# Kernel tuning notes

Measured on AMD Instinct MI355X. Metric: run time of the kernel, lower is better.

## Reference

```python
import jax, jax.numpy as jnp
import numpy as np
import math

F_FEATS = 51
BATCH = 256
N_WINDOW = 10
W_IN = N_WINDOW - 1          # input_window = 9
BUCKET = 6
EMB = 6
HEADS = 3
DHEAD = EMB // HEADS
FFN = 12
TOP_M = 80
HID = F_FEATS * EMB          # 306


def _layernorm(x, s, b, eps=1e-5):
    mu = jnp.mean(x, -1, keepdims=True)
    var = jnp.var(x, -1, keepdims=True)
    return (x - mu) / jnp.sqrt(var + eps) * s + b


def setup_inputs() -> dict:
    key = jax.random.key(0)
    ks = jax.random.split(key, 32)
    g = lambda i, shape, sc=0.1: jax.random.normal(ks[i], shape, dtype=jnp.float32) * sc
    inp = {
        "src": jax.random.uniform(ks[0], (N_WINDOW, BATCH, F_FEATS), dtype=jnp.float32),
        "tgt": jax.random.uniform(ks[1], (N_WINDOW, BATCH, F_FEATS), dtype=jnp.float32),
        # AutoDis params, batched over features (torch loops over n_feats modules)
        "w1_w": g(2, (F_FEATS, BUCKET), 0.5),          # Linear(1,bs) weight squeezed
        "w1_b": g(3, (F_FEATS, BUCKET)),
        "w2_w": g(4, (F_FEATS, BUCKET, BUCKET), 0.3),  # torch layout (out,in)
        "w2_b": g(5, (F_FEATS, BUCKET)),
        "meta": g(6, (F_FEATS, BUCKET, EMB), 0.5),     # EmbeddingBag table per feature
        # Sparse top-m MHSA (1 layer, post-norm encoder)
        "Wq": g(7, (EMB, EMB), 0.3), "bq": g(8, (EMB,)),
        "Wk": g(9, (EMB, EMB), 0.3), "bk": g(10, (EMB,)),
        "Wv": g(11, (EMB, EMB), 0.3), "bv": g(12, (EMB,)),
        "Wo": g(13, (EMB, EMB), 0.3), "bo": g(14, (EMB,)),
        "ln1_s": jnp.ones((EMB,), jnp.float32), "ln1_b": jnp.zeros((EMB,), jnp.float32),
        "ffn_w1": g(15, (FFN, EMB), 0.3), "ffn_b1": g(16, (FFN,)),
        "ffn_w2": g(17, (EMB, FFN), 0.3), "ffn_b2": g(18, (EMB,)),
        "ln2_s": jnp.ones((EMB,), jnp.float32), "ln2_b": jnp.zeros((EMB,), jnp.float32),
        # GRU (1 layer), torch gate order r,z,n
        "gru_wih": g(19, (3 * HID, HID), 0.05),
        "gru_whh": g(20, (3 * HID, HID), 0.05),
        "gru_bih": g(21, (3 * HID,)),
        "gru_bhh": g(22, (3 * HID,)),
        "h0": g(23, (1, BATCH, HID), 1.0),             # init_hidden
        # final FCN
        "fcn_w": g(24, (F_FEATS, HID), 0.05),
        "fcn_b": g(25, (F_FEATS,)),
    }
    return inp


def reference(src, tgt, w1_w, w1_b, w2_w, w2_b, meta,
              Wq, bq, Wk, bk, Wv, bv, Wo, bo,
              ln1_s, ln1_b, ffn_w1, ffn_b1, ffn_w2, ffn_b2, ln2_s, ln2_b,
              gru_wih, gru_whh, gru_bih, gru_bhh, h0, fcn_w, fcn_b):
    s = src[:-1]                                  # [W=9, B, F]
    W, B, F = s.shape
    # ---- AutoDis, vectorized across all features (replaces per-feature loop) ----
    h1 = jax.nn.leaky_relu(s[..., None] * w1_w + w1_b)            # [W,B,F,6]
    h2 = jnp.einsum('wbfi,fji->wbfj', h1, w2_w) + w2_b            # Linear(bs,bs)
    probs = jax.nn.softmax((h2 + 0.5 * h1) / 1e-5, axis=-1)      # temperature 1e-5
    emb = jnp.einsum('wbfi,fie->wbfe', probs, meta)               # weighted EmbeddingBag sum
    # rearrange 'w b f e -> b (w f) e' and scale by sqrt(emb)
    x = emb.transpose(1, 0, 2, 3).reshape(B, W * F, EMB) * math.sqrt(EMB)
    # ---- Sparse top-m MHSA encoder layer (post-norm) ----
    T = W * F                                                     # 459 tokens
    def heads(t):
        return t.reshape(B, T, HEADS, DHEAD).transpose(0, 2, 1, 3)
    q = heads(x @ Wq.T + bq)
    k = heads(x @ Wk.T + bk)
    v = heads(x @ Wv.T + bv)
    scores = jnp.einsum('bhqd,bhkd->bhqk', q, k) / math.sqrt(DHEAD)
    kth = jax.lax.top_k(scores, TOP_M)[0][..., -1:]               # m-th largest per query
    scores = jnp.where(scores >= kth, scores, -jnp.inf)           # keep only top-m keys
    attn = jax.nn.softmax(scores, axis=-1)
    o = jnp.einsum('bhqk,bhkd->bhqd', attn, v).transpose(0, 2, 1, 3).reshape(B, T, EMB)
    x = _layernorm(x + (o @ Wo.T + bo), ln1_s, ln1_b)
    f = jax.nn.relu(x @ ffn_w1.T + ffn_b1) @ ffn_w2.T + ffn_b2
    x = _layernorm(x + f, ln2_s, ln2_b)
    # rearrange 'b (w f) e -> w b (f e)'
    seq = x.reshape(B, W, F, EMB).transpose(1, 0, 2, 3).reshape(W, B, F * EMB)
    # ---- GRU over seq[:-1] (8 steps) ----
    def step(h, xt):
        gi = xt @ gru_wih.T + gru_bih
        gh = h @ gru_whh.T + gru_bhh
        ir, iz, inn = jnp.split(gi, 3, -1)
        hr, hz, hn = jnp.split(gh, 3, -1)
        r = jax.nn.sigmoid(ir + hr)
        z = jax.nn.sigmoid(iz + hz)
        n = jnp.tanh(inn + r * hn)
        h = (1.0 - z) * n + z * h
        return h, None
    hT, _ = jax.lax.scan(step, h0[0, :B], seq[:-1])               # lstm_out[-1] == final hidden
    out = jax.nn.sigmoid(hT @ fcn_w.T + fcn_b)[None]              # [1, B, F]
    return out


if __name__ == '__main__':
    o = reference(**setup_inputs())
    print(o.shape)
```

## Files before the change

kernel.cpp:

```cpp
#include <hip/hip_runtime.h>
#include <math.h>

#define WWIN 9
#define BATCH 256
#define FEAT 51
#define TT 459
#define EMBD 6
#define HID 306
#define G3 918
#define FFND 12
#define TOPM 80
#define MAXTASK 320
#define NPAIR 153
#define NPAIR2 154
#define WSTRIDE 920

__device__ __forceinline__ float leakyf(float v){ return v >= 0.f ? v : 0.01f*v; }
__device__ __forceinline__ float sigmf(float v){ return 1.f/(1.f+__expf(-v)); }

__device__ __forceinline__ unsigned fkey(float s){
    unsigned fb = __float_as_uint(s);
    unsigned m = (unsigned)((int)fb >> 31);
    return fb ^ (m | 0x80000000u);
}
__device__ __forceinline__ float fkey_inv(unsigned k){
    unsigned fb = (k & 0x80000000u) ? (k ^ 0x80000000u) : ~k;
    return __uint_as_float(fb);
}
__device__ __forceinline__ unsigned bfrne(float f){
    unsigned u = __float_as_uint(f);
    u += 0x7fffu + ((u >> 16) & 1u);
    return u >> 16;
}

template<int CTRL, int RMASK>
__device__ __forceinline__ float dpp_add(float v){
    int r = __builtin_amdgcn_update_dpp(0, __float_as_int(v), CTRL, RMASK, 0xf, true);
    return v + __int_as_float(r);
}
__device__ __forceinline__ float wave_fsum(float v){
    v = dpp_add<0x111, 0xf>(v);
    v = dpp_add<0x112, 0xf>(v);
    v = dpp_add<0x114, 0xf>(v);
    v = dpp_add<0x118, 0xf>(v);
    v = dpp_add<0x142, 0xa>(v);
    v = dpp_add<0x143, 0xc>(v);
    return __int_as_float(__builtin_amdgcn_readlane(__float_as_int(v), 63));
}
template<int CTRL, int RMASK>
__device__ __forceinline__ unsigned dpp_uadd(unsigned v){
    unsigned r = (unsigned)__builtin_amdgcn_update_dpp(0, (int)v, CTRL, RMASK, 0xf, true);
    return v + r;
}
__device__ __forceinline__ unsigned wave_usum(unsigned v){
    v = dpp_uadd<0x111, 0xf>(v);
    v = dpp_uadd<0x112, 0xf>(v);
    v = dpp_uadd<0x114, 0xf>(v);
    v = dpp_uadd<0x118, 0xf>(v);
    v = dpp_uadd<0x142, 0xa>(v);
    v = dpp_uadd<0x143, 0xc>(v);
    return (unsigned)__builtin_amdgcn_readlane((int)v, 63);
}
template<int CTRL, int RMASK>
__device__ __forceinline__ unsigned dpp_min(unsigned v){
    unsigned r = (unsigned)__builtin_amdgcn_update_dpp((int)v, (int)v, CTRL, RMASK, 0xf, false);
    return v < r ? v : r;
}
__device__ __forceinline__ unsigned wave_umin(unsigned v){
    v = dpp_min<0x111, 0xf>(v);
    v = dpp_min<0x112, 0xf>(v);
    v = dpp_min<0x114, 0xf>(v);
    v = dpp_min<0x118, 0xf>(v);
    v = dpp_min<0x142, 0xa>(v);
    v = dpp_min<0x143, 0xc>(v);
    return (unsigned)__builtin_amdgcn_readlane((int)v, 63);
}

__global__ __launch_bounds__(512) void embed_tasks(
    const float* __restrict__ src,
    const float* __restrict__ w1w, const float* __restrict__ w1b,
    const float* __restrict__ w2w, const float* __restrict__ w2b,
    const float* __restrict__ meta,
    const float* __restrict__ Wq, const float* __restrict__ bq,
    const float* __restrict__ Wk, const float* __restrict__ bk,
    const float* __restrict__ Wv, const float* __restrict__ bv,
    const float* __restrict__ wih, const float* __restrict__ whh,
    const float* __restrict__ fcw,
    float* __restrict__ WIHT, unsigned* __restrict__ WHB, float* __restrict__ FCNT,
    float* __restrict__ X, float* __restrict__ Q,
    float* __restrict__ K, float* __restrict__ V,
    int* __restrict__ TASKS, int* __restrict__ ROWMAP, int* __restrict__ NT)
{
    __shared__ int sbuck[TT];
    int b = blockIdx.x;
    int t = threadIdx.x;

    for (int idx = blockIdx.x*512 + threadIdx.x; idx < G3*HID; idx += 256*512){
        int o = idx / HID, i = idx % HID;
        WIHT[i*G3 + o] = wih[idx];
    }
    for (int idx = blockIdx.x*512 + threadIdx.x; idx < NPAIR2*WSTRIDE; idx += 256*512){
        int p = idx / WSTRIDE, c = idx % WSTRIDE;
        unsigned v = 0u;
        if (c < G3 && p < NPAIR){
            unsigned lo = bfrne(whh[(size_t)c*HID + 2*p]);
            unsigned hi = bfrne(whh[(size_t)c*HID + 2*p + 1]);
            v = lo | (hi << 16);
        }
        WHB[idx] = v;
    }
    for (int idx = blockIdx.x*512 + threadIdx.x; idx < FEAT*HID; idx += 256*512){
        int f = idx / HID, i = idx % HID;
        FCNT[i*FEAT + f] = fcw[idx];
    }

    if (t < TT){
        int w = t / FEAT, f = t % FEAT;
        float s = src[(w*BATCH + b)*FEAT + f];
        float h1[EMBD], h2[EMBD];
        #pragma unroll
        for (int i=0;i<EMBD;i++) h1[i] = leakyf(s*w1w[f*EMBD+i] + w1b[f*EMBD+i]);
        #pragma unroll
        for (int j=0;j<EMBD;j++){
            float a = 0.f;
            #pragma unroll
            for (int i=0;i<EMBD;i++) a += h1[i]*w2w[(f*EMBD+j)*EMBD+i];
            h2[j] = a + w2b[f*EMBD+j];
        }
        float z[EMBD];
        float m = -INFINITY; int jm = 0;
        #pragma unroll
        for (int j=0;j<EMBD;j++){
            z[j] = (h2[j] + 0.5f*h1[j]) * 1e+05f;
            if (z[j] > m){ m = z[j]; jm = j; }
        }
        float se = 0.f;
        #pragma unroll
        for (int j=0;j<EMBD;j++){ z[j] = expf(z[j]-m); se += z[j]; }
        float inv = 1.0f / se;
        #pragma unroll
        for (int j=0;j<EMBD;j++) z[j] *= inv;
        sbuck[t] = jm;

        float xr[EMBD];
        #pragma unroll
        for (int e=0;e<EMBD;e++){
            float a = 0.f;
            #pragma unroll
            for (int i=0;i<EMBD;i++) a += z[i]*meta[(f*EMBD+i)*EMBD+e];
            xr[e] = a * 2.449489742783178f;
        }
        float* xp = X + (b*TT + t)*EMBD;
        float* qp = Q + (b*TT + t)*EMBD;
        float* kp = K + (b*TT + t)*EMBD;
        float* vp = V + (b*TT + t)*EMBD;
        #pragma unroll
        for (int e=0;e<EMBD;e++){
            xp[e] = xr[e];
            float aq=0.f, ak=0.f, av=0.f;
            #pragma unroll
            for (int i=0;i<EMBD;i++){
                aq += xr[i]*Wq[e*EMBD+i];
                ak += xr[i]*Wk[e*EMBD+i];
                av += xr[i]*Wv[e*EMBD+i];
            }
            qp[e] = aq + bq[e];
            kp[e] = ak + bk[e];
            vp[e] = av + bv[e];
        }
    }
    __syncthreads();
    if (threadIdx.x < 64){
        int f = threadIdx.x;
        unsigned mask = 0; unsigned cnts = 0; int repw[6]; int cnt = 0;
        if (f < FEAT){
            #pragma unroll
            for (int w=0; w<WWIN; w++){
                int j = sbuck[w*FEAT + f];
                if (!((mask>>j) & 1u)){ mask |= 1u<<j; repw[j] = w; }
                cnts += 1u << (5*j);
            }
            cnt = __popc(mask);
        }
        int inc = cnt;
        #pragma unroll
        for (int off=1; off<64; off<<=1){
            int n = __shfl_up(inc, off, 64);
            if (threadIdx.x >= off) inc += n;
        }
        int offset = inc - cnt;
        if (f < FEAT){
            int rk = 0;
            #pragma unroll
            for (int j=0;j<6;j++){
                if ((mask>>j) & 1u){
                    int mult = (int)((cnts >> (5*j)) & 31u);
                    TASKS[b*MAXTASK + offset + rk] =
                        (mult<<13) | (f<<7) | (j<<4) | repw[j];
                    rk++;
                }
            }
            #pragma unroll
            for (int w=0;w<WWIN;w++){
                int j = sbuck[w*FEAT + f];
                int r = __popc(mask & ((1u<<j)-1u));
                ROWMAP[b*TT + w*FEAT + f] = offset + r;
            }
        }
        if (threadIdx.x == 63) NT[b] = inc;
    }
}

__global__ __launch_bounds__(256) void attn_topk(
    const float* __restrict__ Q, const float* __restrict__ K,
    const float* __restrict__ V, const int* __restrict__ TASKS,
    const int* __restrict__ NT, float2* __restrict__ OD)
{
    int blk = blockIdx.x;
    int b = blk / 3, h = blk % 3;
    const int base = b*TT*EMBD + 2*h;
    int wave = threadIdx.x >> 6, lane = threadIdx.x & 63;
    int nt = NT[b];

    float rkx[4], rky[4], rvx[4], rvy[4], rmf[4];
    unsigned rpm[4];
    #pragma unroll
    for (int s=0;s<4;s++){
        int tix = lane + (s<<6);
        rkx[s]=0.f; rky[s]=0.f; rvx[s]=0.f; rvy[s]=0.f; rmf[s]=0.f; rpm[s]=0u;
        if (tix < nt){
            int pk = TASKS[b*MAXTASK + tix];
            int rep_t = (pk & 15)*FEAT + ((pk >> 7) & 63);
            int mult = pk >> 13;
            rkx[s] = K[base + rep_t*EMBD];
            rky[s] = K[base + rep_t*EMBD + 1];
            rvx[s] = V[base + rep_t*EMBD];
            rvy[s] = V[base + rep_t*EMBD + 1];
            rmf[s] = (float)mult;
            rpm[s] = ((unsigned)mult << 10) | 1u;
        }
    }

    const float SC = 0.7071067811865476f;
    for (int idx = blockIdx.y*4 + wave; idx < nt; idx += 16){
        int pk = TASKS[b*MAXTASK + idx];
        int rep_t = (pk & 15)*FEAT + ((pk >> 7) & 63);
        float q0 = Q[base + rep_t*EMBD]     * SC;
        float q1 = Q[base + rep_t*EMBD + 1] * SC;

        float sv[4]; unsigned uk[4];
        #pragma unroll
        for (int s=0;s<4;s++){
            float sc = q0*rkx[s] + q1*rky[s];
            sv[s] = sc;
            uk[s] = rpm[s] ? fkey(sc) : 0u;
        }
        unsigned T = 0;
        int Dwin = nt, Dabove = 0;
        int mode = 0; unsigned Ue = 0;
        for (int bit = 31; bit >= 0; --bit){
            unsigned Tp = T | (1u<<bit);
            unsigned acc = 0;
            #pragma unroll
            for (int s=0;s<4;s++) acc += (uk[s] >= Tp) ? rpm[s] : 0u;
            acc = wave_usum(acc);
            int cw = (int)(acc >> 10);
            int dg = (int)(acc & 1023u);
            int dhi = dg - Dabove;
            if (cw >= TOPM){
                T = Tp; Dwin = dhi;
                if (cw == TOPM){ mode = 1; break; }
            } else {
                Dwin -= dhi; Dabove = dg;
            }
            if (Dwin == 1){ mode = 2; Ue = T + (1u<<bit); break; }
        }
        if (mode == 0)      Ue = T + 1u;
        else if (mode == 1) Ue = 0xFFFFFFFFu;
        unsigned mn = 0xFFFFFFFFu;
        #pragma unroll
        for (int s=0;s<4;s++){
            unsigned cand = (rpm[s] && uk[s] >= T && uk[s] < Ue) ? uk[s] : 0xFFFFFFFFu;
            mn = min(mn, cand);
        }
        unsigned kth = wave_umin(mn);
        float skth = fkey_inv(kth);
        float den=0.f, ox=0.f, oy=0.f;
        #pragma unroll
        for (int s=0;s<4;s++){
            float p = __expf(sv[s] - skth) * rmf[s];
            p = (uk[s] >= kth) ? p : 0.f;
            den += p; ox += p*rvx[s]; oy += p*rvy[s];
        }
        den = wave_fsum(den);
        ox  = wave_fsum(ox);
        oy  = wave_fsum(oy);
        if (lane == 0){
            float id = 1.0f/den;
            OD[(b*3 + h)*MAXTASK + idx] = make_float2(ox*id, oy*id);
        }
    }
}

__global__ __launch_bounds__(256) void post_gi(
    const float* __restrict__ X, const float2* __restrict__ OD,
    const int* __restrict__ ROWMAP,
    const float* __restrict__ Wo, const float* __restrict__ bo,
    const float* __restrict__ l1s, const float* __restrict__ l1b,
    const float* __restrict__ fw1, const float* __restrict__ fb1,
    const float* __restrict__ fw2, const float* __restrict__ fb2,
    const float* __restrict__ l2s, const float* __restrict__ l2b,
    const float* __restrict__ WIHT, const float* __restrict__ bih,
    float* __restrict__ GI)
{
    __shared__ float sL[8][HID];
    int gy = blockIdx.y, gx = blockIdx.x;
    for (int idx = threadIdx.x; idx < 8*FEAT; idx += 256){
        int k = idx / FEAT, ff = idx % FEAT;
        int r = gy*8 + k;
        int w = r >> 8, b = r & 255;
        int t = w*FEAT + ff;
        const float* xr = X + (b*TT + t)*EMBD;
        int rm = ROWMAP[b*TT + t];
        float orow[EMBD];
        #pragma unroll
        for (int h=0;h<3;h++){
            float2 od = OD[(b*3 + h)*MAXTASK + rm];
            orow[2*h]   = od.x;
            orow[2*h+1] = od.y;
        }
        float y[EMBD];
        #pragma unroll
        for (int e=0;e<EMBD;e++){
            float a = 0.f;
            #pragma unroll
            for (int e2=0;e2<EMBD;e2++) a += orow[e2]*Wo[e*EMBD+e2];
            y[e] = xr[e] + a + bo[e];
        }
        float mu=0.f;
        #pragma unroll
        for (int e=0;e<EMBD;e++) mu += y[e];
        mu *= (1.f/6.f);
        float var=0.f;
        #pragma unroll
        for (int e=0;e<EMBD;e++){ float d = y[e]-mu; var += d*d; }
        var *= (1.f/6.f);
        float isd = 1.0f / sqrtf(var + 1e-05f);
        float xn[EMBD];
        #pragma unroll
        for (int e=0;e<EMBD;e++) xn[e] = (y[e]-mu)*isd*l1s[e] + l1b[e];
        float hd[FFND];
        #pragma unroll
        for (int kk2=0;kk2<FFND;kk2++){
            float a = fb1[kk2];
            #pragma unroll
            for (int e=0;e<EMBD;e++) a += xn[e]*fw1[kk2*EMBD+e];
            hd[kk2] = fmaxf(a, 0.f);
        }
        float y2[EMBD];
        #pragma unroll
        for (int e=0;e<EMBD;e++){
            float a = fb2[e];
            #pragma unroll
            for (int kk2=0;kk2<FFND;kk2++) a += hd[kk2]*fw2[e*FFND+kk2];
            y2[e] = xn[e] + a;
        }
        float mu2=0.f;
        #pragma unroll
        for (int e=0;e<EMBD;e++) mu2 += y2[e];
        mu2 *= (1.f/6.f);
        float var2=0.f;
        #pragma unroll
        for (int e=0;e<EMBD;e++){ float d = y2[e]-mu2; var2 += d*d; }
        var2 *= (1.f/6.f);
        float isd2 = 1.0f / sqrtf(var2 + 1e-05f);
        #pragma unroll
        for (int e=0;e<EMBD;e++) sL[k][ff*EMBD+e] = (y2[e]-mu2)*isd2*l2s[e] + l2b[e];
    }
    __syncthreads();
    int col = gx*256 + threadIdx.x;
    if (col >= G3) return;
    float acc[8];
    #pragma unroll
    for (int k=0;k<8;k++) acc[k] = 0.f;
    for (int i=0;i<HID;i++){
        float wv = WIHT[i*G3 + col];
        #pragma unroll
        for (int k=0;k<8;k++) acc[k] += sL[k][i]*wv;
    }
    float bb = bih[col];
    #pragma unroll
    for (int k=0;k<8;k++) GI[(size_t)(gy*8+k)*G3 + col] = acc[k] + bb;
}

#define PFR 3

#define LOADR(buf, c_) { \
    int p0_ = pbase + (c_)*PFR; \
    _Pragma("unroll") \
    for (int r=0;r<PFR;r++){ \
        const unsigned* wp = WHB + (size_t)(p0_+r)*WSTRIDE + jc; \
        buf[3*r] = wp[0]; buf[3*r+1] = wp[HID]; buf[3*r+2] = wp[2*HID]; \
    } }

#define COMPR(buf, c_) { \
    int p0_ = pbase + (c_)*PFR; \
    _Pragma("unroll") \
    for (int r=0;r<PFR;r++){ \
        float2 h2 = *(const float2*)&hL[2*(p0_+r)]; \
        unsigned pr_ = buf[3*r], pz_ = buf[3*r+1], pn_ = buf[3*r+2]; \
        float wr0 = __uint_as_float(pr_ << 16), wr1 = __uint_as_float(pr_ & 0xffff0000u); \
        float wz0 = __uint_as_float(pz_ << 16), wz1 = __uint_as_float(pz_ & 0xffff0000u); \
        float wn0 = __uint_as_float(pn_ << 16), wn1 = __uint_as_float(pn_ & 0xffff0000u); \
        ar = fmaf(wr0, h2.x, fmaf(wr1, h2.y, ar)); \
        az = fmaf(wz0, h2.x, fmaf(wz1, h2.y, az)); \
        an = fmaf(wn0, h2.x, fmaf(wn1, h2.y, an)); \
    } }

__global__ __launch_bounds__(960) void gru_fcn(
    const float* __restrict__ GI, const unsigned* __restrict__ WHB,
    const float* __restrict__ bhh, const float* __restrict__ h0,
    const float* __restrict__ FCNT, const float* __restrict__ fcb,
    float* __restrict__ out)
{
    __shared__ float hL[HID + 2];
    __shared__ float pB[2*HID*3];
    int b = blockIdx.x;
    int tid = threadIdx.x;
    if (tid < HID) hL[tid] = h0[(size_t)b*HID + tid];
    if (tid >= HID && tid < HID+2) hL[tid] = 0.f;
    __syncthreads();

    int s = tid / 320;
    int j = tid - s*320;
    bool act = (j < HID);
    int jc = act ? j : 0;
    int pbase = s*51;
    float br=0.f, bz=0.f, bn=0.f;
    if (s == 0 && act){ br = bhh[j]; bz = bhh[HID+j]; bn = bhh[2*HID+j]; }

    for (int step = 0; step < 8; ++step){
        float gr=0.f, gz=0.f, gn=0.f;
        if (s == 0 && act){
            const float* gi = GI + ((size_t)step*BATCH + b)*G3;
            gr = gi[j]; gz = gi[HID+j]; gn = gi[2*HID+j];
        }
        float ar = 0.f, az = 0.f, an = 0.f;
        unsigned bufA[3*PFR], bufB[3*PFR];
        LOADR(bufA, 0);
        #pragma unroll 1
        for (int p = 0; p < 8; ++p){
            LOADR(bufB, 2*p+1);
            COMPR(bufA, 2*p);
            LOADR(bufA, 2*p+2);
            COMPR(bufB, 2*p+1);
        }
        COMPR(bufA, 16);
        float hold = (s == 0) ? hL[jc] : 0.f;
        if (s > 0 && act){
            int base = ((s-1)*HID + j)*3;
            pB[base] = ar; pB[base+1] = az; pB[base+2] = an;
        }
        __syncthreads();
        if (s == 0 && act){
            float a2r = pB[j*3],       a2z = pB[j*3+1],       a2n = pB[j*3+2];
            float a3r = pB[(HID+j)*3], a3z = pB[(HID+j)*3+1], a3n = pB[(HID+j)*3+2];
            float rr = sigmf(gr + ar + a2r + a3r + br);
            float zz = sigmf(gz + az + a2z + a3z + bz);
            float nn = tanhf(gn + rr*(an + a2n + a3n + bn));
            hL[j] = (1.f - zz)*nn + zz*hold;
        }
        __syncthreads();
    }

    if (tid < FEAT){
        int f = tid;
        float acc = 0.f;
        #pragma unroll 6
        for (int i=0;i<HID;i++) acc += hL[i]*FCNT[i*FEAT+f];
        out[(size_t)b*FEAT + f] = sigmf(acc + fcb[f]);
    }
}

extern "C" void kernel_launch(void* const* d_in, const int* in_sizes, int n_in,
                              void* d_out, int out_size, void* d_ws, size_t ws_size,
                              hipStream_t stream)
{
    const float* src = (const float*)d_in[0];
    const float* w1w = (const float*)d_in[2];
    const float* w1b = (const float*)d_in[3];
    const float* w2w = (const float*)d_in[4];
    const float* w2b = (const float*)d_in[5];
    const float* meta= (const float*)d_in[6];
    const float* Wq = (const float*)d_in[7];  const float* bq = (const float*)d_in[8];
    const float* Wk = (const float*)d_in[9];  const float* bk = (const float*)d_in[10];
    const float* Wv = (const float*)d_in[11]; const float* bv = (const float*)d_in[12];
    const float* Wo = (const float*)d_in[13]; const float* bo = (const float*)d_in[14];
    const float* l1s= (const float*)d_in[15]; const float* l1b= (const float*)d_in[16];
    const float* fw1= (const float*)d_in[17]; const float* fb1= (const float*)d_in[18];
    const float* fw2= (const float*)d_in[19]; const float* fb2= (const float*)d_in[20];
    const float* l2s= (const float*)d_in[21]; const float* l2b= (const float*)d_in[22];
    const float* wih= (const float*)d_in[23]; const float* whh= (const float*)d_in[24];
    const float* bih= (const float*)d_in[25]; const float* bhh= (const float*)d_in[26];
    const float* h0 = (const float*)d_in[27];
    const float* fcw= (const float*)d_in[28]; const float* fcb= (const float*)d_in[29];

    float* ws = (float*)d_ws;
    float* X    = ws;
    float* Q    = X    + 705024;
    float* K    = Q    + 705024;
    float* V    = K    + 705024;
    float* GI   = V    + 705024;
    float* WIHT = GI   + 1880064;
    unsigned* WHB = (unsigned*)(WIHT + 280908);
    float* FCNT = (float*)(WHB + 141680);
    float* ODf  = FCNT + 15606;
    int*   TASKS= (int*)(ODf + 491520);
    int*   RMAP = TASKS + 81920;
    int*   NT   = RMAP + 117504;
    float2* OD  = (float2*)ODf;
    float* outp = (float*)d_out;

    embed_tasks<<<256, 512, 0, stream>>>(src, w1w, w1b, w2w, w2b, meta,
                                         Wq,bq,Wk,bk,Wv,bv, wih, whh, fcw,
                                         WIHT, WHB, FCNT,
                                         X,Q,K,V, TASKS, RMAP, NT);
    {
        dim3 g(768, 4);
        attn_topk<<<g, 256, 0, stream>>>(Q, K, V, TASKS, NT, OD);
    }
    {
        dim3 g(4, 256);
        post_gi<<<g, 256, 0, stream>>>(X, OD, RMAP, Wo, bo, l1s, l1b,
                                       fw1, fb1, fw2, fb2, l2s, l2b,
                                       WIHT, bih, GI);
    }
    gru_fcn<<<256, 960, 0, stream>>>(GI, WHB, bhh, h0, FCNT, fcb, outp);
}
```

Before: 186.1 us.

## Split GRU recurrence into per-step launches sharing weights across four batch rows

The single persistent GRU kernel, one block per batch row with 960 threads, is replaced by eight per-step launches. Each launch uses 256 blocks, and each block handles four batch rows and a quarter of the hidden columns, so every bf16 weight load is reused across four hidden states. The final FCN runs as a separate small kernel. This cuts total weight-read traffic by about four times, at the cost of eight extra kernel launches and hidden state passing through global memory between steps.

```diff
diff --git a/kernel.cpp b/kernel.cpp
--- a/kernel.cpp
+++ b/kernel.cpp
@@ -14,6 +14,7 @@
 #define NPAIR 153
 #define NPAIR2 154
 #define WSTRIDE 920
+#define JSW 77
 
 __device__ __forceinline__ float leakyf(float v){ return v >= 0.f ? v : 0.01f*v; }
 __device__ __forceinline__ float sigmf(float v){ return 1.f/(1.f+__expf(-v)); }
@@ -395,7 +396,7 @@
 
 #define PFR 3
 
-#define LOADR(buf, c_) { \
+#define LOADS(buf, c_) { \
     int p0_ = pbase + (c_)*PFR; \
     _Pragma("unroll") \
     for (int r=0;r<PFR;r++){ \
@@ -403,83 +404,97 @@
         buf[3*r] = wp[0]; buf[3*r+1] = wp[HID]; buf[3*r+2] = wp[2*HID]; \
     } }
 
-#define COMPR(buf, c_) { \
+#define COMPS(buf, c_) { \
     int p0_ = pbase + (c_)*PFR; \
     _Pragma("unroll") \
     for (int r=0;r<PFR;r++){ \
-        float2 h2 = *(const float2*)&hL[2*(p0_+r)]; \
         unsigned pr_ = buf[3*r], pz_ = buf[3*r+1], pn_ = buf[3*r+2]; \
         float wr0 = __uint_as_float(pr_ << 16), wr1 = __uint_as_float(pr_ & 0xffff0000u); \
         float wz0 = __uint_as_float(pz_ << 16), wz1 = __uint_as_float(pz_ & 0xffff0000u); \
         float wn0 = __uint_as_float(pn_ << 16), wn1 = __uint_as_float(pn_ & 0xffff0000u); \
-        ar = fmaf(wr0, h2.x, fmaf(wr1, h2.y, ar)); \
-        az = fmaf(wz0, h2.x, fmaf(wz1, h2.y, az)); \
-        an = fmaf(wn0, h2.x, fmaf(wn1, h2.y, an)); \
+        _Pragma("unroll") \
+        for (int q=0;q<4;q++){ \
+            float2 h2 = *(const float2*)&hL[q*308 + 2*(p0_+r)]; \
+            ar[q] = fmaf(wr0, h2.x, fmaf(wr1, h2.y, ar[q])); \
+            az[q] = fmaf(wz0, h2.x, fmaf(wz1, h2.y, az[q])); \
+            an[q] = fmaf(wn0, h2.x, fmaf(wn1, h2.y, an[q])); \
+        } \
     } }
 
-__global__ __launch_bounds__(960) void gru_fcn(
-    const float* __restrict__ GI, const unsigned* __restrict__ WHB,
-    const float* __restrict__ bhh, const float* __restrict__ h0,
-    const float* __restrict__ FCNT, const float* __restrict__ fcb,
-    float* __restrict__ out)
+__global__ __launch_bounds__(256) void gru_step(
+    const float* __restrict__ GIstep, const unsigned* __restrict__ WHB,
+    const float* __restrict__ bhh, const float* __restrict__ HP,
+    float* __restrict__ HN)
 {
-    __shared__ float hL[HID + 2];
-    __shared__ float pB[2*HID*3];
+    __shared__ float hL[4*308];
+    __shared__ float pB[2*JSW*13];
+    int js = blockIdx.x & 3;
+    int b0 = (blockIdx.x >> 2) * 4;
+    int tid = threadIdx.x;
+    for (int idx = tid; idx < 4*HID; idx += 256){
+        int q = idx / HID, i = idx % HID;
+        hL[q*308 + i] = HP[(size_t)(b0+q)*HID + i];
+    }
+    __syncthreads();
+
+    int is = tid / JSW;
+    int cl = tid - is*JSW;
+    int c  = js*JSW + cl;
+    bool act = (is < 3) && (c < HID);
+    int jc = act ? c : 0;
+    int pbase = act ? is*51 : 0;
+
+    float ar[4]={0,0,0,0}, az[4]={0,0,0,0}, an[4]={0,0,0,0};
+    unsigned bufA[3*PFR], bufB[3*PFR];
+    LOADS(bufA, 0);
+    #pragma unroll 1
+    for (int p = 0; p < 8; ++p){
+        LOADS(bufB, 2*p+1);
+        COMPS(bufA, 2*p);
+        LOADS(bufA, 2*p+2);
+        COMPS(bufB, 2*p+1);
+    }
+    COMPS(bufA, 16);
+
+    if (act && is > 0){
+        int base = ((is-1)*JSW + cl)*13;
+        #pragma unroll
+        for (int q=0;q<4;q++){
+            pB[base + q*3 + 0] = ar[q];
+            pB[base + q*3 + 1] = az[q];
+            pB[base + q*3 + 2] = an[q];
+        }
+    }
+    __syncthreads();
+    if (act && is == 0){
+        float bvr = bhh[c], bvz = bhh[HID+c], bvn = bhh[2*HID+c];
+        #pragma unroll
+        for (int q=0;q<4;q++){
+            const float* gi = GIstep + (size_t)(b0+q)*G3;
+            int b1 = (cl)*13 + q*3;
+            int b2 = (JSW + cl)*13 + q*3;
+            float rr = sigmf(gi[c]       + ar[q] + pB[b1+0] + pB[b2+0] + bvr);
+            float zz = sigmf(gi[HID+c]   + az[q] + pB[b1+1] + pB[b2+1] + bvz);
+            float nn = tanhf(gi[2*HID+c] + rr*(an[q] + pB[b1+2] + pB[b2+2] + bvn));
+            HN[(size_t)(b0+q)*HID + c] = (1.f - zz)*nn + zz*hL[q*308 + c];
+        }
+    }
+}
+
+__global__ __launch_bounds__(64) void fcn_out(
+    const float* __restrict__ H, const float* __restrict__ FCNT,
+    const float* __restrict__ fcb, float* __restrict__ out)
+{
+    __shared__ float hr[HID];
     int b = blockIdx.x;
-    int tid = threadIdx.x;
-    if (tid < HID) hL[tid] = h0[(size_t)b*HID + tid];
-    if (tid >= HID && tid < HID+2) hL[tid] = 0.f;
+    for (int i = threadIdx.x; i < HID; i += 64) hr[i] = H[(size_t)b*HID + i];
     __syncthreads();
-
-    int s = tid / 320;
-    int j = tid - s*320;
-    bool act = (j < HID);
-    int jc = act ? j : 0;
-    int pbase = s*51;
-    float br=0.f, bz=0.f, bn=0.f;
-    if (s == 0 && act){ br = bhh[j]; bz = bhh[HID+j]; bn = bhh[2*HID+j]; }
-
-    for (int step = 0; step < 8; ++step){
-        float gr=0.f, gz=0.f, gn=0.f;
-        if (s == 0 && act){
-            const float* gi = GI + ((size_t)step*BATCH + b)*G3;
-            gr = gi[j]; gz = gi[HID+j]; gn = gi[2*HID+j];
-        }
-        float ar = 0.f, az = 0.f, an = 0.f;
-        unsigned bufA[3*PFR], bufB[3*PFR];
-        LOADR(bufA, 0);
-        #pragma unroll 1
-        for (int p = 0; p < 8; ++p){
-            LOADR(bufB, 2*p+1);
-            COMPR(bufA, 2*p);
-            LOADR(bufA, 2*p+2);
-            COMPR(bufB, 2*p+1);
-        }
-        COMPR(bufA, 16);
-        float hold = (s == 0) ? hL[jc] : 0.f;
-        if (s > 0 && act){
-            int base = ((s-1)*HID + j)*3;
-            pB[base] = ar; pB[base+1] = az; pB[base+2] = an;
-        }
-        __syncthreads();
-        if (s == 0 && act){
-            float a2r = pB[j*3],       a2z = pB[j*3+1],       a2n = pB[j*3+2];
-            float a3r = pB[(HID+j)*3], a3z = pB[(HID+j)*3+1], a3n = pB[(HID+j)*3+2];
-            float rr = sigmf(gr + ar + a2r + a3r + br);
-            float zz = sigmf(gz + az + a2z + a3z + bz);
-            float nn = tanhf(gn + rr*(an + a2n + a3n + bn));
-            hL[j] = (1.f - zz)*nn + zz*hold;
-        }
-        __syncthreads();
-    }
-
-    if (tid < FEAT){
-        int f = tid;
-        float acc = 0.f;
-        #pragma unroll 6
-        for (int i=0;i<HID;i++) acc += hL[i]*FCNT[i*FEAT+f];
-        out[(size_t)b*FEAT + f] = sigmf(acc + fcb[f]);
-    }
+    int f = threadIdx.x;
+    if (f >= FEAT) return;
+    float acc = 0.f;
+    #pragma unroll 6
+    for (int i=0;i<HID;i++) acc += hr[i]*FCNT[i*FEAT+f];
+    out[(size_t)b*FEAT + f] = sigmf(acc + fcb[f]);
 }
 
 extern "C" void kernel_launch(void* const* d_in, const int* in_sizes, int n_in,
@@ -518,6 +533,8 @@
     int*   TASKS= (int*)(ODf + 491520);
     int*   RMAP = TASKS + 81920;
     int*   NT   = RMAP + 117504;
+    float* HA   = (float*)(NT + 256);
+    float* HB   = HA + 78336;
     float2* OD  = (float2*)ODf;
     float* outp = (float*)d_out;
 
@@ -535,5 +552,12 @@
                                        fw1, fb1, fw2, fb2, l2s, l2b,
                                        WIHT, bih, GI);
     }
-    gru_fcn<<<256, 960, 0, stream>>>(GI, WHB, bhh, h0, FCNT, fcb, outp);
-}
+    const float* hp = h0;
+    float* hbufs[2] = {HA, HB};
+    for (int t = 0; t < 8; ++t){
+        float* hn = hbufs[t & 1];
+        gru_step<<<256, 256, 0, stream>>>(GI + (size_t)t*BATCH*G3, WHB, bhh, hp, hn);
+        hp = hn;
+    }
+    fcn_out<<<256, 64, 0, stream>>>(hp, FCNT, fcb, outp);
+}
```

After: 222.2 us. +19.4%, slower.

## Merge post_gi column blocks so each block computes all GI columns once

Applied to the files above, without the earlier changes.

The post_gi launch drops from a 4x256 grid to 256 blocks, and each thread now accumulates four column slices of the 918-wide GI row for 8 rows. Before, each of the 4 column blocks recomputed the same attention-output/layernorm/FFN prologue for its 8 rows. The shared tile is transposed to [HID][8], so the row values come from two float4 LDS reads per input index. This removes the 4x redundant prologue work and cuts shared-memory reads. The cost is 32 accumulators per thread and only 256 blocks, which lowers parallelism for the GEMM part.

```diff
diff --git a/kernel.cpp b/kernel.cpp
--- a/kernel.cpp
+++ b/kernel.cpp
@@ -313,8 +313,8 @@
     const float* __restrict__ WIHT, const float* __restrict__ bih,
     float* __restrict__ GI)
 {
-    __shared__ float sL[8][HID];
-    int gy = blockIdx.y, gx = blockIdx.x;
+    __shared__ float sL[HID][8];
+    int gy = blockIdx.x;
     for (int idx = threadIdx.x; idx < 8*FEAT; idx += 256){
         int k = idx / FEAT, ff = idx % FEAT;
         int r = gy*8 + k;
@@ -375,22 +375,48 @@
         var2 *= (1.f/6.f);
         float isd2 = 1.0f / sqrtf(var2 + 1e-05f);
         #pragma unroll
-        for (int e=0;e<EMBD;e++) sL[k][ff*EMBD+e] = (y2[e]-mu2)*isd2*l2s[e] + l2b[e];
+        for (int e=0;e<EMBD;e++) sL[ff*EMBD+e][k] = (y2[e]-mu2)*isd2*l2s[e] + l2b[e];
     }
     __syncthreads();
-    int col = gx*256 + threadIdx.x;
-    if (col >= G3) return;
-    float acc[8];
+
+    int c0 = threadIdx.x;
+    bool has3 = (c0 + 768) < G3;
+    float a0[8], a1[8], a2[8], a3[8];
     #pragma unroll
-    for (int k=0;k<8;k++) acc[k] = 0.f;
+    for (int k=0;k<8;k++){ a0[k]=0.f; a1[k]=0.f; a2[k]=0.f; a3[k]=0.f; }
     for (int i=0;i<HID;i++){
-        float wv = WIHT[i*G3 + col];
-        #pragma unroll
-        for (int k=0;k<8;k++) acc[k] += sL[k][i]*wv;
-    }
-    float bb = bih[col];
+        float4 hA = *(const float4*)&sL[i][0];
+        float4 hB = *(const float4*)&sL[i][4];
+        const float* wr = WIHT + (size_t)i*G3 + c0;
+        float w0 = wr[0], w1 = wr[256], w2 = wr[512];
+        float w3 = has3 ? wr[768] : 0.f;
+        a0[0] = fmaf(w0,hA.x,a0[0]); a0[1] = fmaf(w0,hA.y,a0[1]);
+        a0[2] = fmaf(w0,hA.z,a0[2]); a0[3] = fmaf(w0,hA.w,a0[3]);
+        a0[4] = fmaf(w0,hB.x,a0[4]); a0[5] = fmaf(w0,hB.y,a0[5]);
+        a0[6] = fmaf(w0,hB.z,a0[6]); a0[7] = fmaf(w0,hB.w,a0[7]);
+        a1[0] = fmaf(w1,hA.x,a1[0]); a1[1] = fmaf(w1,hA.y,a1[1]);
+        a1[2] = fmaf(w1,hA.z,a1[2]); a1[3] = fmaf(w1,hA.w,a1[3]);
+        a1[4] = fmaf(w1,hB.x,a1[4]); a1[5] = fmaf(w1,hB.y,a1[5]);
+        a1[6] = fmaf(w1,hB.z,a1[6]); a1[7] = fmaf(w1,hB.w,a1[7]);
+        a2[0] = fmaf(w2,hA.x,a2[0]); a2[1] = fmaf(w2,hA.y,a2[1]);
+        a2[2] = fmaf(w2,hA.z,a2[2]); a2[3] = fmaf(w2,hA.w,a2[3]);
+        a2[4] = fmaf(w2,hB.x,a2[4]); a2[5] = fmaf(w2,hB.y,a2[5]);
+        a2[6] = fmaf(w2,hB.z,a2[6]); a2[7] = fmaf(w2,hB.w,a2[7]);
+        a3[0] = fmaf(w3,hA.x,a3[0]); a3[1] = fmaf(w3,hA.y,a3[1]);
+        a3[2] = fmaf(w3,hA.z,a3[2]); a3[3] = fmaf(w3,hA.w,a3[3]);
+        a3[4] = fmaf(w3,hB.x,a3[4]); a3[5] = fmaf(w3,hB.y,a3[5]);
+        a3[6] = fmaf(w3,hB.z,a3[6]); a3[7] = fmaf(w3,hB.w,a3[7]);
+    }
+    float b0v = bih[c0], b1v = bih[c0+256], b2v = bih[c0+512];
+    float b3v = has3 ? bih[c0+768] : 0.f;
     #pragma unroll
-    for (int k=0;k<8;k++) GI[(size_t)(gy*8+k)*G3 + col] = acc[k] + bb;
+    for (int k=0;k<8;k++){
+        size_t row = (size_t)(gy*8 + k)*G3;
+        GI[row + c0]       = a0[k] + b0v;
+        GI[row + c0 + 256] = a1[k] + b1v;
+        GI[row + c0 + 512] = a2[k] + b2v;
+        if (has3) GI[row + c0 + 768] = a3[k] + b3v;
+    }
 }
 
 #define PFR 3
@@ -529,11 +555,8 @@
         dim3 g(768, 4);
         attn_topk<<<g, 256, 0, stream>>>(Q, K, V, TASKS, NT, OD);
     }
-    {
-        dim3 g(4, 256);
-        post_gi<<<g, 256, 0, stream>>>(X, OD, RMAP, Wo, bo, l1s, l1b,
-                                       fw1, fb1, fw2, fb2, l2s, l2b,
-                                       WIHT, bih, GI);
-    }
+    post_gi<<<256, 256, 0, stream>>>(X, OD, RMAP, Wo, bo, l1s, l1b,
+                                     fw1, fb1, fw2, fb2, l2s, l2b,
+                                     WIHT, bih, GI);
     gru_fcn<<<256, 960, 0, stream>>>(GI, WHB, bhh, h0, FCNT, fcb, outp);
 }
```

Measured after the change: 192.7 us. 3.5% more time.

## Register-tile input-gate GEMM with float4 weight loads and padded layout

Applied to the files above, without the earlier changes.

The post-attention input-gate projection is restructured so that each thread computes a 4-column by 4-row tile, with float4 loads from a transposed W_ih whose row stride is padded to 920. The staging buffer in shared memory becomes row-interleaved [HID][4], so one float4 read supplies all four rows. The grid changes from 4x256 blocks to 512 one-dimensional blocks that each cover every column, which removes the repeated layer-norm/FFN prologue that the column-split blocks used to redo. The cost is that the whole weight matrix is now read once per 4 rows instead of once per 8, which doubles L2 weight traffic. The workspace gains padding so the float4 reads past the last row stay in bounds.

```diff
diff --git a/kernel.cpp b/kernel.cpp
--- a/kernel.cpp
+++ b/kernel.cpp
@@ -14,6 +14,7 @@
 #define NPAIR 153
 #define NPAIR2 154
 #define WSTRIDE 920
+#define WIHS 920
 
 __device__ __forceinline__ float leakyf(float v){ return v >= 0.f ? v : 0.01f*v; }
 __device__ __forceinline__ float sigmf(float v){ return 1.f/(1.f+__expf(-v)); }
@@ -97,7 +98,7 @@
 
     for (int idx = blockIdx.x*512 + threadIdx.x; idx < G3*HID; idx += 256*512){
         int o = idx / HID, i = idx % HID;
-        WIHT[i*G3 + o] = wih[idx];
+        WIHT[(size_t)i*WIHS + o] = wih[idx];
     }
     for (int idx = blockIdx.x*512 + threadIdx.x; idx < NPAIR2*WSTRIDE; idx += 256*512){
         int p = idx / WSTRIDE, c = idx % WSTRIDE;
@@ -313,11 +314,11 @@
     const float* __restrict__ WIHT, const float* __restrict__ bih,
     float* __restrict__ GI)
 {
-    __shared__ float sL[8][HID];
-    int gy = blockIdx.y, gx = blockIdx.x;
-    for (int idx = threadIdx.x; idx < 8*FEAT; idx += 256){
+    __shared__ __align__(16) float sL[HID][4];
+    int gy = blockIdx.x;
+    for (int idx = threadIdx.x; idx < 4*FEAT; idx += 256){
         int k = idx / FEAT, ff = idx % FEAT;
-        int r = gy*8 + k;
+        int r = gy*4 + k;
         int w = r >> 8, b = r & 255;
         int t = w*FEAT + ff;
         const float* xr = X + (b*TT + t)*EMBD;
@@ -375,22 +376,39 @@
         var2 *= (1.f/6.f);
         float isd2 = 1.0f / sqrtf(var2 + 1e-05f);
         #pragma unroll
-        for (int e=0;e<EMBD;e++) sL[k][ff*EMBD+e] = (y2[e]-mu2)*isd2*l2s[e] + l2b[e];
+        for (int e=0;e<EMBD;e++) sL[ff*EMBD+e][k] = (y2[e]-mu2)*isd2*l2s[e] + l2b[e];
     }
     __syncthreads();
-    int col = gx*256 + threadIdx.x;
-    if (col >= G3) return;
-    float acc[8];
+
+    int c0 = threadIdx.x * 4;
+    float a0[4], a1[4], a2[4], a3[4];
     #pragma unroll
-    for (int k=0;k<8;k++) acc[k] = 0.f;
+    for (int k=0;k<4;k++){ a0[k]=0.f; a1[k]=0.f; a2[k]=0.f; a3[k]=0.f; }
+    #pragma unroll 4
     for (int i=0;i<HID;i++){
-        float wv = WIHT[i*G3 + col];
-        #pragma unroll
-        for (int k=0;k<8;k++) acc[k] += sL[k][i]*wv;
-    }
-    float bb = bih[col];
+        float4 hv = *(const float4*)&sL[i][0];
+        float4 wv = *(const float4*)(WIHT + (size_t)i*WIHS + c0);
+        a0[0] = fmaf(wv.x,hv.x,a0[0]); a0[1] = fmaf(wv.x,hv.y,a0[1]);
+        a0[2] = fmaf(wv.x,hv.z,a0[2]); a0[3] = fmaf(wv.x,hv.w,a0[3]);
+        a1[0] = fmaf(wv.y,hv.x,a1[0]); a1[1] = fmaf(wv.y,hv.y,a1[1]);
+        a1[2] = fmaf(wv.y,hv.z,a1[2]); a1[3] = fmaf(wv.y,hv.w,a1[3]);
+        a2[0] = fmaf(wv.z,hv.x,a2[0]); a2[1] = fmaf(wv.z,hv.y,a2[1]);
+        a2[2] = fmaf(wv.z,hv.z,a2[2]); a2[3] = fmaf(wv.z,hv.w,a2[3]);
+        a3[0] = fmaf(wv.w,hv.x,a3[0]); a3[1] = fmaf(wv.w,hv.y,a3[1]);
+        a3[2] = fmaf(wv.w,hv.z,a3[2]); a3[3] = fmaf(wv.w,hv.w,a3[3]);
+    }
     #pragma unroll
-    for (int k=0;k<8;k++) GI[(size_t)(gy*8+k)*G3 + col] = acc[k] + bb;
+    for (int c=0;c<4;c++){
+        int col = c0 + c;
+        if (col < G3){
+            float bb = bih[col];
+            const float* av = (c==0)?a0:(c==1)?a1:(c==2)?a2:a3;
+            #pragma unroll
+            for (int k=0;k<4;k++){
+                GI[(size_t)(gy*4 + k)*G3 + col] = av[k] + bb;
+            }
+        }
+    }
 }
 
 #define PFR 3
@@ -512,7 +530,7 @@
     float* V    = K    + 705024;
     float* GI   = V    + 705024;
     float* WIHT = GI   + 1880064;
-    unsigned* WHB = (unsigned*)(WIHT + 280908);
+    unsigned* WHB = (unsigned*)(WIHT + 281520 + 128);
     float* FCNT = (float*)(WHB + 141680);
     float* ODf  = FCNT + 15606;
     int*   TASKS= (int*)(ODf + 491520);
@@ -529,11 +547,8 @@
         dim3 g(768, 4);
         attn_topk<<<g, 256, 0, stream>>>(Q, K, V, TASKS, NT, OD);
     }
-    {
-        dim3 g(4, 256);
-        post_gi<<<g, 256, 0, stream>>>(X, OD, RMAP, Wo, bo, l1s, l1b,
-                                       fw1, fb1, fw2, fb2, l2s, l2b,
-                                       WIHT, bih, GI);
-    }
+    post_gi<<<512, 256, 0, stream>>>(X, OD, RMAP, Wo, bo, l1s, l1b,
+                                     fw1, fb1, fw2, fb2, l2s, l2b,
+                                     WIHT, bih, GI);
     gru_fcn<<<256, 960, 0, stream>>>(GI, WHB, bhh, h0, FCNT, fcb, outp);
 }
```

New measurement: 194.9 us. +4.7%, slower.
